# Kernel tuning notes

Measured on AMD Instinct MI355X. Metric: run time of the kernel, lower is better.

## Reference

```python
import jax, jax.numpy as jnp
import numpy as np

D_MODEL = 1024
N_HEADS = 16
D_HEAD = D_MODEL // N_HEADS
QLEN = 512
MLEN = 512
BATCH = 8


def setup_inputs() -> dict:
    key = jax.random.key(0)
    ks = jax.random.split(key, 12)
    s = 0.02
    inputs = jax.random.normal(ks[0], (QLEN, BATCH, D_MODEL), jnp.float32)
    r = jax.random.normal(ks[1], (QLEN + MLEN, 1, D_MODEL), jnp.float32)
    u = jax.random.normal(ks[2], (N_HEADS, D_HEAD), jnp.float32) * s
    v = jax.random.normal(ks[3], (N_HEADS, D_HEAD), jnp.float32) * s
    mem = jax.random.normal(ks[4], (MLEN, BATCH, D_MODEL), jnp.float32)
    # attention params (Transformer-XL style): fused qkv, r-projection, output proj
    W_qkv = jax.random.normal(ks[5], (D_MODEL, 3 * D_MODEL), jnp.float32) * s
    W_r = jax.random.normal(ks[6], (D_MODEL, D_MODEL), jnp.float32) * s
    W_o = jax.random.normal(ks[7], (D_MODEL, D_MODEL), jnp.float32) * s
    # GRU params: input-hidden and hidden-hidden for gates (r, z, n), torch layout
    W_ih = jax.random.normal(ks[8], (3 * D_MODEL, D_MODEL), jnp.float32) * s
    W_hh = jax.random.normal(ks[9], (3 * D_MODEL, D_MODEL), jnp.float32) * s
    b_ih = jax.random.normal(ks[10], (3 * D_MODEL,), jnp.float32) * s
    b_hh = jax.random.normal(ks[11], (3 * D_MODEL,), jnp.float32) * s
    h0 = jnp.zeros((BATCH, D_MODEL), jnp.float32)
    return dict(inputs=inputs, r=r, u=u, v=v, mem=mem, W_qkv=W_qkv, W_r=W_r,
                W_o=W_o, W_ih=W_ih, W_hh=W_hh, b_ih=b_ih, b_hh=b_hh, h0=h0)


def _rel_shift(x):
    # x: [q, k, b, h] -> Transformer-XL relative shift
    q, k, b, h = x.shape
    zero_pad = jnp.zeros((q, 1, b, h), x.dtype)
    x_padded = jnp.concatenate([zero_pad, x], axis=1)        # [q, k+1, b, h]
    x_padded = x_padded.reshape(k + 1, q, b, h)
    return x_padded[1:].reshape(q, k, b, h)


def _attention(inputs, r, u, v, mem, W_qkv, W_r, W_o):
    qlen, bsz, _ = inputs.shape
    cat = jnp.concatenate([mem, inputs], axis=0)             # [klen, b, d]
    klen = cat.shape[0]
    qkv = cat @ W_qkv                                        # [klen, b, 3d]
    w_head_q, w_head_k, w_head_v = jnp.split(qkv, 3, axis=-1)
    w_head_q = w_head_q[-qlen:]                              # [q, b, d]
    r_head_k = (r[:, 0, :] @ W_r).reshape(klen, N_HEADS, D_HEAD)  # [k, h, dh]

    q_ = w_head_q.reshape(qlen, bsz, N_HEADS, D_HEAD)
    k_ = w_head_k.reshape(klen, bsz, N_HEADS, D_HEAD)
    v_ = w_head_v.reshape(klen, bsz, N_HEADS, D_HEAD)

    AC = jnp.einsum('ibhd,jbhd->ijbh', q_ + u[None, None], k_)
    BD = jnp.einsum('ibhd,jhd->ijbh', q_ + v[None, None], r_head_k)
    BD = _rel_shift(BD)
    scale = 1.0 / np.sqrt(D_HEAD)
    attn_score = (AC + BD) * scale                           # [q, k, b, h]

    # causal mask with memory: query i attends to keys j <= i + mlen
    mlen = klen - qlen
    i = jnp.arange(qlen)[:, None]
    j = jnp.arange(klen)[None, :]
    mask = j > (i + mlen)                                    # [q, k]
    attn_score = jnp.where(mask[:, :, None, None], -jnp.inf, attn_score)

    attn_prob = jax.nn.softmax(attn_score, axis=1)
    attn_vec = jnp.einsum('ijbh,jbhd->ibhd', attn_prob, v_)
    attn_vec = attn_vec.reshape(qlen, bsz, D_MODEL)
    return attn_vec @ W_o                                    # [q, b, d]


def _gru(x, h0, W_ih, W_hh, b_ih, b_hh):
    # x: [T, B, D]; torch GRU cell math
    Wi_r, Wi_z, Wi_n = jnp.split(W_ih, 3, axis=0)
    Wh_r, Wh_z, Wh_n = jnp.split(W_hh, 3, axis=0)
    bi_r, bi_z, bi_n = jnp.split(b_ih, 3)
    bh_r, bh_z, bh_n = jnp.split(b_hh, 3)

    # precompute input projections for all timesteps
    xr = x @ Wi_r.T + bi_r
    xz = x @ Wi_z.T + bi_z
    xn = x @ Wi_n.T + bi_n

    def step(h, xs):
        xr_t, xz_t, xn_t = xs
        r = jax.nn.sigmoid(xr_t + h @ Wh_r.T + bh_r)
        z = jax.nn.sigmoid(xz_t + h @ Wh_z.T + bh_z)
        n = jnp.tanh(xn_t + r * (h @ Wh_n.T + bh_n))
        h_new = (1.0 - z) * n + z * h
        return h_new, h_new

    _, ys = jax.lax.scan(step, h0, (xr, xz, xn))
    return ys                                                # [T, B, D]


def reference(inputs, r, u, v, mem, W_qkv, W_r, W_o, W_ih, W_hh, b_ih, b_hh, h0):
    y = _attention(inputs, r, u, v, mem, W_qkv, W_r, W_o)
    return _gru(y, h0, W_ih, W_hh, b_ih, b_hh)
```

## Files before the change

kernel.cpp:

```cpp
#include <hip/hip_runtime.h>
#include <math.h>


typedef short bf16x8 __attribute__((ext_vector_type(8)));
typedef float f32x4 __attribute__((ext_vector_type(4)));

union FragU { uint4 u; bf16x8 h; };

__device__ inline void split2(float x0, float x1, unsigned& hi, unsigned& lo) {
    unsigned u0 = __float_as_uint(x0), u1 = __float_as_uint(x1);
    float h0 = __uint_as_float(u0 & 0xffff0000u);
    float h1 = __uint_as_float(u1 & 0xffff0000u);
    unsigned l0 = __float_as_uint(x0 - h0), l1 = __float_as_uint(x1 - h1);
    hi = (u0 >> 16) | (u1 & 0xffff0000u);
    lo = (l0 >> 16) | (l1 & 0xffff0000u);
}

__device__ __forceinline__ unsigned long long ld_coh64(const void* p) {
    return __hip_atomic_load((const unsigned long long*)p, __ATOMIC_RELAXED,
                             __HIP_MEMORY_SCOPE_AGENT);
}
__device__ __forceinline__ void st_coh64(void* p, unsigned long long v) {
    __hip_atomic_store((unsigned long long*)p, v, __ATOMIC_RELAXED,
                       __HIP_MEMORY_SCOPE_AGENT);
}

__device__ __forceinline__ void gl_lds16(const uint4* g, uint4* l) {
    __builtin_amdgcn_global_load_lds(
        (const __attribute__((address_space(1))) uint4*)g,
        (__attribute__((address_space(3))) uint4*)l, 16, 0, 0);
}

template<bool TR>
__global__ __launch_bounds__(256) void prep_w(
    const float* __restrict__ W, unsigned* __restrict__ out, int Nr, int K, int ldw)
{
    int idx = blockIdx.x * 256 + threadIdx.x;
    int cpr = K >> 3;
    if (idx >= Nr * cpr) return;
    int n, c;
    if (TR) { n = idx % Nr; c = idx / Nr; }
    else    { c = idx % cpr; n = idx / cpr; }
    int kt = c >> 2, j = c & 3;
    int k = kt * 32 + j * 8;
    float x[8];
    #pragma unroll
    for (int i = 0; i < 8; ++i)
        x[i] = TR ? W[(size_t)(k + i) * ldw + n] : W[(size_t)n * ldw + k + i];
    unsigned h[4], l[4];
    split2(x[0], x[1], h[0], l[0]);
    split2(x[2], x[3], h[1], l[1]);
    split2(x[4], x[5], h[2], l[2]);
    split2(x[6], x[7], h[3], l[3]);
    unsigned* base = out + (size_t)n * K + kt * 32;
    *(uint4*)(base + (((2 * j) ^ (n & 7)) * 4))     = make_uint4(h[0], h[1], h[2], h[3]);
    *(uint4*)(base + (((2 * j + 1) ^ (n & 7)) * 4)) = make_uint4(l[0], l[1], l[2], l[3]);
}

__global__ __launch_bounds__(256) void prep_cat(
    const float* __restrict__ mem, const float* __restrict__ inputs,
    unsigned* __restrict__ out)
{
    int idx = blockIdx.x * 256 + threadIdx.x;
    if (idx >= 1048576) return;
    int c = idx & 127, n = idx >> 7;
    int kt = c >> 2, j = c & 3;
    int k = kt * 32 + j * 8;
    const float* src = (n < 4096) ? (mem + (size_t)n * 1024 + k)
                                  : (inputs + (size_t)(n - 4096) * 1024 + k);
    float4 x0 = *(const float4*)src, x1 = *(const float4*)(src + 4);
    unsigned h[4], l[4];
    split2(x0.x, x0.y, h[0], l[0]);
    split2(x0.z, x0.w, h[1], l[1]);
    split2(x1.x, x1.y, h[2], l[2]);
    split2(x1.z, x1.w, h[3], l[3]);
    unsigned* base = out + (size_t)n * 1024 + kt * 32;
    *(uint4*)(base + (((2 * j) ^ (n & 7)) * 4))     = make_uint4(h[0], h[1], h[2], h[3]);
    *(uint4*)(base + (((2 * j + 1) ^ (n & 7)) * 4)) = make_uint4(l[0], l[1], l[2], l[3]);
}

template<bool BIAS>
__global__ __launch_bounds__(256) void gemm_pp(
    const uint4* __restrict__ Ap4, const uint4* __restrict__ Bp4,
    const float* __restrict__ bias, float* __restrict__ C, int K, int ldc)
{
    __shared__ uint4 Ab[1024];
    __shared__ uint4 Bb[1024];
    int tid = threadIdx.x;
    int lane = tid & 63, wid = tid >> 6;
    int wr = wid >> 1, wc = wid & 1;
    int n0 = blockIdx.x * 128, m0 = blockIdx.y * 128;
    int r15 = lane & 15, s = lane >> 4;
    int K4 = K >> 2;

    f32x4 acc[4][4];
    #pragma unroll
    for (int i = 0; i < 4; ++i)
        #pragma unroll
        for (int j = 0; j < 4; ++j) acc[i][j] = 0.0f;

    for (int kt = 0; kt < (K >> 5); ++kt) {
        #pragma unroll
        for (int q = 0; q < 4; ++q) {
            int base = q * 256 + wid * 64;
            int idx  = base + lane;
            int row = idx >> 3, slot = idx & 7;
            gl_lds16(Ap4 + (size_t)(m0 + row) * K4 + kt * 8 + slot, &Ab[base]);
            gl_lds16(Bp4 + (size_t)(n0 + row) * K4 + kt * 8 + slot, &Bb[base]);
        }
        __syncthreads();
        FragU ahi[4], alo[4], bhi[4], blo[4];
        #pragma unroll
        for (int f = 0; f < 4; ++f) {
            int ar = wr * 64 + f * 16 + r15;
            ahi[f].u = Ab[ar * 8 + ((2 * s) ^ (ar & 7))];
            alo[f].u = Ab[ar * 8 + ((2 * s + 1) ^ (ar & 7))];
            int br = wc * 64 + f * 16 + r15;
            bhi[f].u = Bb[br * 8 + ((2 * s) ^ (br & 7))];
            blo[f].u = Bb[br * 8 + ((2 * s + 1) ^ (br & 7))];
        }
        #pragma unroll
        for (int fi = 0; fi < 4; ++fi)
            #pragma unroll
            for (int fj = 0; fj < 4; ++fj) {
                acc[fi][fj] = __builtin_amdgcn_mfma_f32_16x16x32_bf16(ahi[fi].h, bhi[fj].h, acc[fi][fj], 0, 0, 0);
                acc[fi][fj] = __builtin_amdgcn_mfma_f32_16x16x32_bf16(ahi[fi].h, blo[fj].h, acc[fi][fj], 0, 0, 0);
                acc[fi][fj] = __builtin_amdgcn_mfma_f32_16x16x32_bf16(alo[fi].h, bhi[fj].h, acc[fi][fj], 0, 0, 0);
            }
        __syncthreads();
    }
    int r4 = (lane >> 4) * 4;
    #pragma unroll
    for (int fj = 0; fj < 4; ++fj) {
        int n = n0 + wc * 64 + fj * 16 + r15;
        float bv = BIAS ? bias[n] : 0.f;
        #pragma unroll
        for (int fi = 0; fi < 4; ++fi) {
            int m = m0 + wr * 64 + fi * 16 + r4;
            #pragma unroll
            for (int r = 0; r < 4; ++r)
                C[(size_t)(m + r) * ldc + n] = acc[fi][fj][r] + bv;
        }
    }
}

template<int AMODE, bool BIAS>
__global__ __launch_bounds__(256) void gemm_mfma(
    const float* __restrict__ A, const float* __restrict__ A2,
    const unsigned* __restrict__ Bp, const float* __restrict__ bias,
    float* __restrict__ C, int M, int N, int K, int lda, int ldc)
{
    __shared__ uint4 Ab[1024];
    __shared__ uint4 Bb[1024];
    int tid = threadIdx.x;
    int lane = tid & 63, wid = tid >> 6;
    int wr = wid >> 1, wc = wid & 1;
    int n0 = blockIdx.x * 128, m0 = blockIdx.y * 128;
    int r15 = lane & 15, s = lane >> 4;

    f32x4 acc[4][4];
    #pragma unroll
    for (int i = 0; i < 4; ++i)
        #pragma unroll
        for (int j = 0; j < 4; ++j) acc[i][j] = 0.0f;

    for (int kt = 0; kt < (K >> 5); ++kt) {
        int k0 = kt * 32;
        #pragma unroll
        for (int q = 0; q < 2; ++q) {
            int idx = q * 256 + tid;
            int row = idx >> 2, j = idx & 3;
            const float* ap;
            if (AMODE == 1) {
                int gm = m0 + row;
                ap = (gm < 4096) ? (A + (size_t)gm * lda) : (A2 + (size_t)(gm - 4096) * lda);
            } else {
                ap = A + (size_t)(m0 + row) * lda;
            }
            float4 x0 = *(const float4*)(ap + k0 + j * 8);
            float4 x1 = *(const float4*)(ap + k0 + j * 8 + 4);
            unsigned h[4], l[4];
            split2(x0.x, x0.y, h[0], l[0]);
            split2(x0.z, x0.w, h[1], l[1]);
            split2(x1.x, x1.y, h[2], l[2]);
            split2(x1.z, x1.w, h[3], l[3]);
            Ab[row * 8 + (((2 * j) ^ (row & 7)))]     = make_uint4(h[0], h[1], h[2], h[3]);
            Ab[row * 8 + (((2 * j + 1) ^ (row & 7)))] = make_uint4(l[0], l[1], l[2], l[3]);
        }
        #pragma unroll
        for (int q = 0; q < 4; ++q) {
            int idx = q * 256 + tid;
            int row = idx >> 3, slot = idx & 7;
            Bb[idx] = *(const uint4*)(Bp + (size_t)(n0 + row) * K + k0 + slot * 4);
        }
        __syncthreads();
        FragU ahi[4], alo[4], bhi[4], blo[4];
        #pragma unroll
        for (int f = 0; f < 4; ++f) {
            int ar = wr * 64 + f * 16 + r15;
            ahi[f].u = Ab[ar * 8 + ((2 * s) ^ (ar & 7))];
            alo[f].u = Ab[ar * 8 + ((2 * s + 1) ^ (ar & 7))];
            int br = wc * 64 + f * 16 + r15;
            bhi[f].u = Bb[br * 8 + ((2 * s) ^ (br & 7))];
            blo[f].u = Bb[br * 8 + ((2 * s + 1) ^ (br & 7))];
        }
        #pragma unroll
        for (int fi = 0; fi < 4; ++fi)
            #pragma unroll
            for (int fj = 0; fj < 4; ++fj) {
                acc[fi][fj] = __builtin_amdgcn_mfma_f32_16x16x32_bf16(ahi[fi].h, bhi[fj].h, acc[fi][fj], 0, 0, 0);
                acc[fi][fj] = __builtin_amdgcn_mfma_f32_16x16x32_bf16(ahi[fi].h, blo[fj].h, acc[fi][fj], 0, 0, 0);
                acc[fi][fj] = __builtin_amdgcn_mfma_f32_16x16x32_bf16(alo[fi].h, bhi[fj].h, acc[fi][fj], 0, 0, 0);
            }
        __syncthreads();
    }
    int r4 = (lane >> 4) * 4;
    #pragma unroll
    for (int fj = 0; fj < 4; ++fj) {
        int n = n0 + wc * 64 + fj * 16 + r15;
        float bv = BIAS ? bias[n] : 0.f;
        #pragma unroll
        for (int fi = 0; fi < 4; ++fi) {
            int m = m0 + wr * 64 + fi * 16 + r4;
            #pragma unroll
            for (int r = 0; r < 4; ++r)
                C[(size_t)(m + r) * ldc + n] = acc[fi][fj][r] + bv;
        }
    }
}

__global__ __launch_bounds__(256) void attn_fused(
    const float* __restrict__ qkv, const float* __restrict__ rk,
    const float* __restrict__ u_, const float* __restrict__ v_,
    float* __restrict__ y1)
{
    __shared__ float qu[64][68], qv[64][68], Kt[64][68], Vt[64][68];
    __shared__ float RKs[128][68];
    __shared__ float S[64][68];
    __shared__ float mrow[64], lrow[64], scalef[64];
    __shared__ float pmax[64][16], psum[64][16];

    int tid = threadIdx.x;
    int it = blockIdx.x, b = blockIdx.y, h = blockIdx.z;
    int i0 = it * 64;
    int ti = tid >> 4, tj = tid & 15;

    {
        int r = tid >> 2, c0 = (tid & 3) * 16;
        size_t base = ((size_t)(i0 + r + 512) * 8 + b) * 3072 + h * 64;
        #pragma unroll
        for (int q = 0; q < 4; ++q) {
            int c = c0 + q * 4;
            float4 qq = *(const float4*)&qkv[base + c];
            float4 uu = *(const float4*)&u_[h * 64 + c];
            float4 vv = *(const float4*)&v_[h * 64 + c];
            *(float4*)&qu[r][c] = make_float4(qq.x + uu.x, qq.y + uu.y, qq.z + uu.z, qq.w + uu.w);
            *(float4*)&qv[r][c] = make_float4(qq.x + vv.x, qq.y + vv.y, qq.z + vv.z, qq.w + vv.w);
        }
    }
    if (tid < 64) { mrow[tid] = -1e30f; lrow[tid] = 0.f; }

    float Od[4][4] = {};
    int njt = it + 9;

    for (int jt = 0; jt < njt; ++jt) {
        int j0 = jt * 64;
        __syncthreads();
        {
            int r = tid >> 2, c0 = (tid & 3) * 16;
            size_t kb = ((size_t)(j0 + r) * 8 + b) * 3072 + 1024 + h * 64;
            #pragma unroll
            for (int q = 0; q < 4; ++q) {
                int c = c0 + q * 4;
                *(float4*)&Kt[r][c] = *(const float4*)&qkv[kb + c];
                *(float4*)&Vt[r][c] = *(const float4*)&qkv[kb + 1024 + c];
            }
        }
        {
            int r2 = tid >> 1, c0 = (tid & 1) * 32;
            int jj = j0 - i0 + 448 + r2;
            jj = jj < 0 ? 0 : (jj > 1023 ? 1023 : jj);
            size_t rb = (size_t)jj * 1024 + h * 64;
            #pragma unroll
            for (int q = 0; q < 8; ++q) {
                int c = c0 + q * 4;
                *(float4*)&RKs[r2][c] = *(const float4*)&rk[rb + c];
            }
        }
        __syncthreads();

        float acc[4][4] = {};
        int jlb = (tj - ti) * 4 + 60;
        #pragma unroll 4
        for (int d4 = 0; d4 < 64; d4 += 4) {
            float4 Aq[4], Cq[4], Kv[4], Rv[7];
            #pragma unroll
            for (int i = 0; i < 4; ++i) {
                Aq[i] = *(float4*)&qu[ti * 4 + i][d4];
                Cq[i] = *(float4*)&qv[ti * 4 + i][d4];
                Kv[i] = *(float4*)&Kt[tj * 4 + i][d4];
            }
            #pragma unroll
            for (int t = 0; t < 7; ++t)
                Rv[t] = *(float4*)&RKs[jlb + t][d4];
            #pragma unroll
            for (int i = 0; i < 4; ++i)
                #pragma unroll
                for (int j = 0; j < 4; ++j) {
                    float4 kk = Kv[j];
                    float4 rr = Rv[j - i + 3];
                    acc[i][j] += Aq[i].x * kk.x + Aq[i].y * kk.y + Aq[i].z * kk.z + Aq[i].w * kk.w
                               + Cq[i].x * rr.x + Cq[i].y * rr.y + Cq[i].z * rr.z + Cq[i].w * rr.w;
                }
        }
        #pragma unroll
        for (int i = 0; i < 4; ++i) {
            int gi = i0 + ti * 4 + i;
            float mx = -1e30f;
            #pragma unroll
            for (int j = 0; j < 4; ++j) {
                int gj = j0 + tj * 4 + j;
                float vS = acc[i][j] * 0.125f;
                if (gj > gi + 512) vS = -1e30f;
                acc[i][j] = vS;
                mx = fmaxf(mx, vS);
            }
            pmax[ti * 4 + i][tj] = mx;
        }
        __syncthreads();
        if (tid < 64) {
            float mo = mrow[tid], mn = mo;
            #pragma unroll
            for (int t = 0; t < 16; ++t) mn = fmaxf(mn, pmax[tid][t]);
            mrow[tid] = mn;
            scalef[tid] = __expf(mo - mn);
        }
        __syncthreads();
        #pragma unroll
        for (int i = 0; i < 4; ++i) {
            int ri = ti * 4 + i;
            float mn = mrow[ri];
            float4 pv;
            pv.x = __expf(acc[i][0] - mn);
            pv.y = __expf(acc[i][1] - mn);
            pv.z = __expf(acc[i][2] - mn);
            pv.w = __expf(acc[i][3] - mn);
            *(float4*)&S[ri][tj * 4] = pv;
            psum[ri][tj] = pv.x + pv.y + pv.z + pv.w;
            float scl = scalef[ri];
            #pragma unroll
            for (int j2 = 0; j2 < 4; ++j2) Od[i][j2] *= scl;
        }
        __syncthreads();
        if (tid < 64) {
            float s = 0.f;
            #pragma unroll
            for (int t = 0; t < 16; ++t) s += psum[tid][t];
            lrow[tid] = lrow[tid] * scalef[tid] + s;
        }
        #pragma unroll 4
        for (int jb = 0; jb < 64; jb += 4) {
            float4 p0 = *(float4*)&S[ti * 4 + 0][jb];
            float4 p1 = *(float4*)&S[ti * 4 + 1][jb];
            float4 p2 = *(float4*)&S[ti * 4 + 2][jb];
            float4 p3 = *(float4*)&S[ti * 4 + 3][jb];
            float4 v0 = *(float4*)&Vt[jb + 0][tj * 4];
            float4 v1 = *(float4*)&Vt[jb + 1][tj * 4];
            float4 v2 = *(float4*)&Vt[jb + 2][tj * 4];
            float4 v3 = *(float4*)&Vt[jb + 3][tj * 4];
            float4 pr[4] = {p0, p1, p2, p3};
            #pragma unroll
            for (int i = 0; i < 4; ++i) {
                Od[i][0] += pr[i].x * v0.x + pr[i].y * v1.x + pr[i].z * v2.x + pr[i].w * v3.x;
                Od[i][1] += pr[i].x * v0.y + pr[i].y * v1.y + pr[i].z * v2.y + pr[i].w * v3.y;
                Od[i][2] += pr[i].x * v0.z + pr[i].y * v1.z + pr[i].z * v2.z + pr[i].w * v3.z;
                Od[i][3] += pr[i].x * v0.w + pr[i].y * v1.w + pr[i].z * v2.w + pr[i].w * v3.w;
            }
        }
    }
    __syncthreads();
    #pragma unroll
    for (int i = 0; i < 4; ++i) {
        int ri = ti * 4 + i;
        float inv = 1.f / lrow[ri];
        float4 o = make_float4(Od[i][0] * inv, Od[i][1] * inv, Od[i][2] * inv, Od[i][3] * inv);
        *(float4*)&y1[((size_t)(i0 + ri) * 8 + b) * 1024 + h * 64 + tj * 4] = o;
    }
}

__global__ __launch_bounds__(256) void prep_whh(
    const float* __restrict__ Whh, uint4* __restrict__ outp)
{
    int idx = blockIdx.x * 256 + threadIdx.x;
    if (idx >= 393216) return;
    int lane = idx & 63;
    int rest = idx >> 6;
    int gate = rest % 3;
    int kt   = (rest / 3) & 31;
    int g64  = rest / 96;
    int n = gate * 1024 + g64 * 16 + (lane & 15);
    int k = kt * 32 + (lane >> 4) * 8;
    const float* src = Whh + (size_t)n * 1024 + k;
    float4 x0 = *(const float4*)src, x1 = *(const float4*)(src + 4);
    unsigned h[4], l[4];
    split2(x0.x, x0.y, h[0], l[0]);
    split2(x0.z, x0.w, h[1], l[1]);
    split2(x1.x, x1.y, h[2], l[2]);
    split2(x1.z, x1.w, h[3], l[3]);
    outp[((size_t)rest * 2 + 0) * 64 + lane] = make_uint4(h[0], h[1], h[2], h[3]);
    outp[((size_t)rest * 2 + 1) * 64 + lane] = make_uint4(l[0], l[1], l[2], l[3]);
}

__global__ __launch_bounds__(256, 1) void gru_persist2(
    const float* __restrict__ h0, float* __restrict__ hA, float* __restrict__ hB,
    const uint4* __restrict__ WhhG, const float* __restrict__ bhh,
    const float* __restrict__ xg, float* __restrict__ out,
    unsigned* __restrict__ flags)
{
    __shared__ uint4 Bf[4096];
    __shared__ float red[3][64][4];
    int tid = threadIdx.x;
    int lane = tid & 63, wv = tid >> 6;
    int g64 = blockIdx.x;

    int col = lane & 15;
    int d0 = g64 * 16 + (lane >> 4) * 4;
    bool act = (wv == 0) && (col < 8);
    float4 br4 = make_float4(0, 0, 0, 0), bz4 = br4, bn4 = br4;
    if (act) {
        br4 = *(const float4*)&bhh[d0];
        bz4 = *(const float4*)&bhh[1024 + d0];
        bn4 = *(const float4*)&bhh[2048 + d0];
    }
    const uint4* wb = WhhG + (size_t)g64 * 12288 + (wv < 3 ? wv : 0) * 128 + lane;

    for (int t = 0; t < 512; ++t) {
        const float* hi_ = (t == 0) ? h0 : ((t & 1) ? hA : hB);
        float* ho = (t & 1) ? hB : hA;

        float4 xr4, xz4, xn4;
        unsigned long long hp01 = 0, hp23 = 0;
        if (act) {
            size_t xb = ((size_t)t * 8 + col) * 3072 + d0;
            xr4 = *(const float4*)&xg[xb];
            xz4 = *(const float4*)&xg[xb + 1024];
            xn4 = *(const float4*)&xg[xb + 2048];
            hp01 = ld_coh64(hi_ + col * 1024 + d0);
            hp23 = ld_coh64(hi_ + col * 1024 + d0 + 2);
        }

        uint4 wA[16], wB[16];
        #pragma unroll
        for (int q = 0; q < 8; ++q) {
            wA[2 * q]     = wb[q * 384];
            wA[2 * q + 1] = wb[q * 384 + 64];
        }

        unsigned long long hq[16];
        #pragma unroll
        for (int i = 0; i < 4; ++i) {
            int s = i * 256 + tid;
            const float* hp = hi_ + (s & 7) * 1024 + (s >> 5) * 32 + ((s >> 3) & 3) * 8;
            #pragma unroll
            for (int q = 0; q < 4; ++q) hq[i * 4 + q] = ld_coh64(hp + q * 2);
        }
        #pragma unroll
        for (int i = 0; i < 4; ++i) {
            int s = i * 256 + tid;
            int b = s & 7, oct = (s >> 3) & 3, kt = s >> 5;
            float x[8];
            #pragma unroll
            for (int q = 0; q < 4; ++q) {
                x[2 * q]     = __uint_as_float((unsigned)(hq[i * 4 + q] & 0xffffffffu));
                x[2 * q + 1] = __uint_as_float((unsigned)(hq[i * 4 + q] >> 32));
            }
            unsigned hh[4], ll[4];
            split2(x[0], x[1], hh[0], ll[0]);
            split2(x[2], x[3], hh[1], ll[1]);
            split2(x[4], x[5], hh[2], ll[2]);
            split2(x[6], x[7], hh[3], ll[3]);
            int ln = oct * 16 + b;
            Bf[(kt * 2 + 0) * 64 + ln] = make_uint4(hh[0], hh[1], hh[2], hh[3]);
            Bf[(kt * 2 + 1) * 64 + ln] = make_uint4(ll[0], ll[1], ll[2], ll[3]);
        }
        __syncthreads();

        f32x4 acc = 0.0f;
        #define GRU_LOAD(dst, c0)                                   \
            _Pragma("unroll")                                       \
            for (int q = 0; q < 8; ++q) {                           \
                dst[2 * q]     = wb[((c0) * 8 + q) * 384];          \
                dst[2 * q + 1] = wb[((c0) * 8 + q) * 384 + 64];     \
            }
        #define GRU_COMP(src, c0)                                   \
            _Pragma("unroll")                                       \
            for (int q = 0; q < 8; ++q) {                           \
                int kt = (c0) * 8 + q;                              \
                FragU ah, al, bh, bl;                               \
                ah.u = src[2 * q]; al.u = src[2 * q + 1];           \
                bh.u = Bf[(kt * 2 + 0) * 64 + lane];                \
                bl.u = Bf[(kt * 2 + 1) * 64 + lane];                \
                acc = __builtin_amdgcn_mfma_f32_16x16x32_bf16(ah.h, bh.h, acc, 0, 0, 0); \
                acc = __builtin_amdgcn_mfma_f32_16x16x32_bf16(ah.h, bl.h, acc, 0, 0, 0); \
                acc = __builtin_amdgcn_mfma_f32_16x16x32_bf16(al.h, bh.h, acc, 0, 0, 0); \
            }
        if (wv < 3) {
            GRU_LOAD(wB, 1);
            GRU_COMP(wA, 0);
            GRU_LOAD(wA, 2);
            GRU_COMP(wB, 1);
            GRU_LOAD(wB, 3);
            GRU_COMP(wA, 2);
            GRU_COMP(wB, 3);
            *(f32x4*)&red[wv][lane][0] = acc;
        }
        #undef GRU_LOAD
        #undef GRU_COMP
        __syncthreads();

        if (act) {
            f32x4 aR = *(f32x4*)&red[0][lane][0];
            f32x4 aZ = *(f32x4*)&red[1][lane][0];
            f32x4 aN = *(f32x4*)&red[2][lane][0];
            float xr[4] = {xr4.x, xr4.y, xr4.z, xr4.w};
            float xz[4] = {xz4.x, xz4.y, xz4.z, xz4.w};
            float xn[4] = {xn4.x, xn4.y, xn4.z, xn4.w};
            float hp[4] = {__uint_as_float((unsigned)(hp01 & 0xffffffffu)),
                           __uint_as_float((unsigned)(hp01 >> 32)),
                           __uint_as_float((unsigned)(hp23 & 0xffffffffu)),
                           __uint_as_float((unsigned)(hp23 >> 32))};
            float br[4] = {br4.x, br4.y, br4.z, br4.w};
            float bz[4] = {bz4.x, bz4.y, bz4.z, bz4.w};
            float bn[4] = {bn4.x, bn4.y, bn4.z, bn4.w};
            float hn[4];
            #pragma unroll
            for (int r = 0; r < 4; ++r) {
                float rr = 1.f / (1.f + __expf(-(xr[r] + aR[r] + br[r])));
                float zz = 1.f / (1.f + __expf(-(xz[r] + aZ[r] + bz[r])));
                float nn = tanhf(xn[r] + rr * (aN[r] + bn[r]));
                hn[r] = (1.f - zz) * nn + zz * hp[r];
            }
            unsigned long long v01 = (unsigned long long)__float_as_uint(hn[0])
                                   | ((unsigned long long)__float_as_uint(hn[1]) << 32);
            unsigned long long v23 = (unsigned long long)__float_as_uint(hn[2])
                                   | ((unsigned long long)__float_as_uint(hn[3]) << 32);
            st_coh64(ho + col * 1024 + d0, v01);
            st_coh64(ho + col * 1024 + d0 + 2, v23);
            *(float4*)&out[((size_t)t * 8 + col) * 1024 + d0] =
                make_float4(hn[0], hn[1], hn[2], hn[3]);
        }

        if (t != 511) {
            __syncthreads();
            unsigned tgt = (unsigned)t + 1u;
            if (tid < 64) {
                if (tid == 0)
                    __hip_atomic_store(&flags[(size_t)g64 * 16], tgt,
                                       __ATOMIC_RELAXED, __HIP_MEMORY_SCOPE_AGENT);
                const unsigned* fp = &flags[(size_t)tid * 16];
                for (;;) {
                    unsigned f = __hip_atomic_load(fp, __ATOMIC_RELAXED,
                                                   __HIP_MEMORY_SCOPE_AGENT);
                    if (__all(f >= tgt)) break;
                }
            }
            __syncthreads();
        }
    }
}

__global__ __launch_bounds__(192, 1) void gru_step_mfma(
    const float* __restrict__ hin, float* __restrict__ hout,
    const uint4* __restrict__ WhhG, const float* __restrict__ bhh,
    const float* __restrict__ xg, float* __restrict__ out, int t)
{
    __shared__ uint4 Bf[4096];
    __shared__ float red[3][64][4];
    int tid = threadIdx.x;
    int lane = tid & 63, wv = tid >> 6;
    int g64 = blockIdx.x;

    int col = lane & 15;
    int d0 = g64 * 16 + (lane >> 4) * 4;
    bool act = (wv == 0) && (col < 8);
    float4 xr4, xz4, xn4, hp4, br4, bz4, bn4;
    if (act) {
        size_t xb = ((size_t)t * 8 + col) * 3072 + d0;
        xr4 = *(const float4*)&xg[xb];
        xz4 = *(const float4*)&xg[xb + 1024];
        xn4 = *(const float4*)&xg[xb + 2048];
        hp4 = *(const float4*)&hin[col * 1024 + d0];
        br4 = *(const float4*)&bhh[d0];
        bz4 = *(const float4*)&bhh[1024 + d0];
        bn4 = *(const float4*)&bhh[2048 + d0];
    }

    const uint4* wb = WhhG + (size_t)g64 * 12288 + wv * 128 + lane;
    uint4 wA[16], wB[16];
    #pragma unroll
    for (int q = 0; q < 8; ++q) {
        wA[2 * q]     = wb[q * 384];
        wA[2 * q + 1] = wb[q * 384 + 64];
    }

    for (int s = tid; s < 1024; s += 192) {
        int b = s & 7, oct = (s >> 3) & 3, kt = s >> 5;
        const float* hp = hin + b * 1024 + kt * 32 + oct * 8;
        float4 x0 = *(const float4*)hp, x1 = *(const float4*)(hp + 4);
        unsigned hh[4], ll[4];
        split2(x0.x, x0.y, hh[0], ll[0]);
        split2(x0.z, x0.w, hh[1], ll[1]);
        split2(x1.x, x1.y, hh[2], ll[2]);
        split2(x1.z, x1.w, hh[3], ll[3]);
        int ln = oct * 16 + b;
        Bf[(kt * 2 + 0) * 64 + ln] = make_uint4(hh[0], hh[1], hh[2], hh[3]);
        Bf[(kt * 2 + 1) * 64 + ln] = make_uint4(ll[0], ll[1], ll[2], ll[3]);
    }
    __syncthreads();

    f32x4 acc = 0.0f;
    #define GRU_LOAD(dst, c0)                                   \
        _Pragma("unroll")                                       \
        for (int q = 0; q < 8; ++q) {                           \
            dst[2 * q]     = wb[((c0) * 8 + q) * 384];          \
            dst[2 * q + 1] = wb[((c0) * 8 + q) * 384 + 64];     \
        }
    #define GRU_COMP(src, c0)                                   \
        _Pragma("unroll")                                       \
        for (int q = 0; q < 8; ++q) {                           \
            int kt = (c0) * 8 + q;                              \
            FragU ah, al, bh, bl;                               \
            ah.u = src[2 * q]; al.u = src[2 * q + 1];           \
            bh.u = Bf[(kt * 2 + 0) * 64 + lane];                \
            bl.u = Bf[(kt * 2 + 1) * 64 + lane];                \
            acc = __builtin_amdgcn_mfma_f32_16x16x32_bf16(ah.h, bh.h, acc, 0, 0, 0); \
            acc = __builtin_amdgcn_mfma_f32_16x16x32_bf16(ah.h, bl.h, acc, 0, 0, 0); \
            acc = __builtin_amdgcn_mfma_f32_16x16x32_bf16(al.h, bh.h, acc, 0, 0, 0); \
        }
    GRU_LOAD(wB, 1);
    GRU_COMP(wA, 0);
    GRU_LOAD(wA, 2);
    GRU_COMP(wB, 1);
    GRU_LOAD(wB, 3);
    GRU_COMP(wA, 2);
    GRU_COMP(wB, 3);
    #undef GRU_LOAD
    #undef GRU_COMP

    *(f32x4*)&red[wv][lane][0] = acc;
    __syncthreads();

    if (act) {
        f32x4 aR = *(f32x4*)&red[0][lane][0];
        f32x4 aZ = *(f32x4*)&red[1][lane][0];
        f32x4 aN = *(f32x4*)&red[2][lane][0];
        float xr[4] = {xr4.x, xr4.y, xr4.z, xr4.w};
        float xz[4] = {xz4.x, xz4.y, xz4.z, xz4.w};
        float xn[4] = {xn4.x, xn4.y, xn4.z, xn4.w};
        float hp[4] = {hp4.x, hp4.y, hp4.z, hp4.w};
        float br[4] = {br4.x, br4.y, br4.z, br4.w};
        float bz[4] = {bz4.x, bz4.y, bz4.z, bz4.w};
        float bn[4] = {bn4.x, bn4.y, bn4.z, bn4.w};
        float hn[4];
        #pragma unroll
        for (int r = 0; r < 4; ++r) {
            float rr = 1.f / (1.f + __expf(-(xr[r] + aR[r] + br[r])));
            float zz = 1.f / (1.f + __expf(-(xz[r] + aZ[r] + bz[r])));
            float nn = tanhf(xn[r] + rr * (aN[r] + bn[r]));
            hn[r] = (1.f - zz) * nn + zz * hp[r];
        }
        float4 hv = make_float4(hn[0], hn[1], hn[2], hn[3]);
        *(float4*)&hout[col * 1024 + d0] = hv;
        *(float4*)&out[((size_t)t * 8 + col) * 1024 + d0] = hv;
    }
}

extern "C" void kernel_launch(void* const* d_in, const int* in_sizes, int n_in,
                              void* d_out, int out_size, void* d_ws, size_t ws_size,
                              hipStream_t stream) {
    (void)in_sizes; (void)n_in; (void)out_size; (void)ws_size;
    const float* inputs = (const float*)d_in[0];
    const float* r_in   = (const float*)d_in[1];
    const float* u_in   = (const float*)d_in[2];
    const float* v_in   = (const float*)d_in[3];
    const float* mem    = (const float*)d_in[4];
    const float* Wqkv   = (const float*)d_in[5];
    const float* Wr     = (const float*)d_in[6];
    const float* Wo     = (const float*)d_in[7];
    const float* Wih    = (const float*)d_in[8];
    const float* Whh    = (const float*)d_in[9];
    const float* bih    = (const float*)d_in[10];
    const float* bhh    = (const float*)d_in[11];
    const float* h0     = (const float*)d_in[12];
    float* out = (float*)d_out;
    float* ws = (float*)d_ws;

    float*    qkv   = ws;
    float*    rk    = ws + 25165824;
    float*    y1    = ws + 26214400;
    float*    y2    = ws + 30408704;
    float*    xg    = ws + 34603008;
    float*    hA    = ws + 47185920;
    float*    hB    = ws + 47194112;
    unsigned* WqkvP = (unsigned*)(ws + 47202304);
    unsigned* WrP   = (unsigned*)(ws + 50348032);
    unsigned* WoP   = (unsigned*)(ws + 51396608);
    unsigned* WihP  = (unsigned*)(ws + 52445184);
    unsigned* flags = (unsigned*)(ws + 55590912);
    uint4*    WhhG  = (uint4*)qkv;
    unsigned* y1P   = (unsigned*)(qkv + 4194304);
    unsigned* y2P   = (unsigned*)(qkv + 8388608);
    unsigned* catP  = (unsigned*)xg;

    dim3 blk(256);
    prep_w<true ><<<1536, blk, 0, stream>>>(Wqkv, WqkvP, 3072, 1024, 3072);
    prep_w<true ><<< 512, blk, 0, stream>>>(Wr,   WrP,   1024, 1024, 1024);
    prep_w<true ><<< 512, blk, 0, stream>>>(Wo,   WoP,   1024, 1024, 1024);
    prep_w<false><<<1536, blk, 0, stream>>>(Wih,  WihP,  3072, 1024, 1024);
    hipMemsetAsync(flags, 0, 4096, stream);

    prep_cat<<<4096, blk, 0, stream>>>(mem, inputs, catP);
    gemm_pp<false><<<dim3(24, 64), blk, 0, stream>>>(
        (const uint4*)catP, (const uint4*)WqkvP, nullptr, qkv, 1024, 3072);
    gemm_mfma<0, false><<<dim3(8, 8), blk, 0, stream>>>(
        r_in, nullptr, WrP, nullptr, rk, 1024, 1024, 1024, 1024, 1024);
    attn_fused<<<dim3(8, 8, 16), blk, 0, stream>>>(qkv, rk, u_in, v_in, y1);
    prep_whh<<<1536, blk, 0, stream>>>(Whh, WhhG);
    prep_w<false><<<2048, blk, 0, stream>>>(y1, y1P, 4096, 1024, 1024);
    gemm_pp<false><<<dim3(8, 32), blk, 0, stream>>>(
        (const uint4*)y1P, (const uint4*)WoP, nullptr, y2, 1024, 1024);
    prep_w<false><<<2048, blk, 0, stream>>>(y2, y2P, 4096, 1024, 1024);
    gemm_pp<true><<<dim3(24, 32), blk, 0, stream>>>(
        (const uint4*)y2P, (const uint4*)WihP, bih, xg, 1024, 3072);

    {
        const float* a0 = h0; float* a1 = hA; float* a2 = hB;
        const uint4* a3 = WhhG; const float* a4 = bhh; const float* a5 = xg;
        float* a6 = out; unsigned* a7 = flags;
        void* args[8] = {&a0, &a1, &a2, &a3, &a4, &a5, &a6, &a7};
        hipError_t e = hipLaunchCooperativeKernel((void*)gru_persist2,
                                                  dim3(64), dim3(256), args, 0, stream);
        if (e != hipSuccess) {
            const float* hin = h0;
            for (int s = 0; s < 512; ++s) {
                float* hp = (s & 1) ? hB : hA;
                gru_step_mfma<<<64, dim3(192), 0, stream>>>(hin, hp, WhhG, bhh, xg, out, s);
                hin = hp;
            }
        }
    }
}
```

Before: 4.719 ms.

## Fuse bf16 split packing into attention and Wo GEMM epilogues, skip unused QKV work

The attention kernel now writes its output directly in the packed hi/lo bf16 swizzled layout, and the Wo GEMM gains a SPLITOUT epilogue that stages results through shared memory and emits packed output. This removes the two standalone prep_w conversion passes and their intermediate fp32 round trips. The QKV GEMM is split so memory rows compute only K/V columns, skipping the unused Q projection for the memory part. The cost is extra shared-memory syncs in the epilogue and scattered 8-byte stores in attention.

New measurement: 4.701 ms. Within noise of the previous version (-0.4%).

```diff
diff --git a/kernel.cpp b/kernel.cpp
--- a/kernel.cpp
+++ b/kernel.cpp
@@ -79,18 +79,21 @@
     *(uint4*)(base + (((2 * j + 1) ^ (n & 7)) * 4)) = make_uint4(l[0], l[1], l[2], l[3]);
 }
 
-template<bool BIAS>
+template<bool BIAS, bool SPLITOUT>
 __global__ __launch_bounds__(256) void gemm_pp(
     const uint4* __restrict__ Ap4, const uint4* __restrict__ Bp4,
-    const float* __restrict__ bias, float* __restrict__ C, int K, int ldc)
+    const float* __restrict__ bias, float* __restrict__ C,
+    unsigned* __restrict__ Cp, int K, int ldc)
 {
-    __shared__ uint4 Ab[1024];
-    __shared__ uint4 Bb[1024];
+    __shared__ uint4 SH[2048];
+    uint4* Ab = SH;
+    uint4* Bb = SH + 1024;
     int tid = threadIdx.x;
     int lane = tid & 63, wid = tid >> 6;
     int wr = wid >> 1, wc = wid & 1;
     int n0 = blockIdx.x * 128, m0 = blockIdx.y * 128;
     int r15 = lane & 15, s = lane >> 4;
+    int r4 = (lane >> 4) * 4;
     int K4 = K >> 2;
 
     f32x4 acc[4][4];
@@ -129,17 +132,53 @@
             }
         __syncthreads();
     }
-    int r4 = (lane >> 4) * 4;
-    #pragma unroll
-    for (int fj = 0; fj < 4; ++fj) {
-        int n = n0 + wc * 64 + fj * 16 + r15;
-        float bv = BIAS ? bias[n] : 0.f;
-        #pragma unroll
-        for (int fi = 0; fi < 4; ++fi) {
-            int m = m0 + wr * 64 + fi * 16 + r4;
-            #pragma unroll
-            for (int r = 0; r < 4; ++r)
-                C[(size_t)(m + r) * ldc + n] = acc[fi][fj][r] + bv;
+
+    if (!SPLITOUT) {
+        #pragma unroll
+        for (int fj = 0; fj < 4; ++fj) {
+            int n = n0 + wc * 64 + fj * 16 + r15;
+            float bv = BIAS ? bias[n] : 0.f;
+            #pragma unroll
+            for (int fi = 0; fi < 4; ++fi) {
+                int m = m0 + wr * 64 + fi * 16 + r4;
+                #pragma unroll
+                for (int r = 0; r < 4; ++r)
+                    C[(size_t)(m + r) * ldc + n] = acc[fi][fj][r] + bv;
+            }
+        }
+    } else {
+        float* Cs = (float*)SH;
+        #pragma unroll
+        for (int half = 0; half < 2; ++half) {
+            __syncthreads();
+            if (wr == half) {
+                #pragma unroll
+                for (int fi = 0; fi < 4; ++fi)
+                    #pragma unroll
+                    for (int fj = 0; fj < 4; ++fj)
+                        #pragma unroll
+                        for (int r = 0; r < 4; ++r)
+                            Cs[(fi * 16 + r4 + r) * 128 + wc * 64 + fj * 16 + r15] = acc[fi][fj][r];
+            }
+            __syncthreads();
+            #pragma unroll
+            for (int q = 0; q < 4; ++q) {
+                int oc = q * 256 + tid;
+                int lr = oc >> 4, oct = oc & 15;
+                float4 xa = *(float4*)&Cs[lr * 128 + oct * 8];
+                float4 xb = *(float4*)&Cs[lr * 128 + oct * 8 + 4];
+                unsigned hw[4], lw[4];
+                split2(xa.x, xa.y, hw[0], lw[0]);
+                split2(xa.z, xa.w, hw[1], lw[1]);
+                split2(xb.x, xb.y, hw[2], lw[2]);
+                split2(xb.z, xb.w, hw[3], lw[3]);
+                int m = m0 + half * 64 + lr;
+                int k = n0 + oct * 8;
+                int kt2 = k >> 5, j2 = (k >> 3) & 3;
+                unsigned* bp = Cp + (size_t)m * ldc + kt2 * 32;
+                *(uint4*)(bp + (((2 * j2)     ^ (m & 7)) * 4)) = make_uint4(hw[0], hw[1], hw[2], hw[3]);
+                *(uint4*)(bp + (((2 * j2 + 1) ^ (m & 7)) * 4)) = make_uint4(lw[0], lw[1], lw[2], lw[3]);
+            }
         }
     }
 }
@@ -232,7 +271,7 @@
 __global__ __launch_bounds__(256) void attn_fused(
     const float* __restrict__ qkv, const float* __restrict__ rk,
     const float* __restrict__ u_, const float* __restrict__ v_,
-    float* __restrict__ y1)
+    unsigned* __restrict__ y1P)
 {
     __shared__ float qu[64][68], qv[64][68], Kt[64][68], Vt[64][68];
     __shared__ float RKs[128][68];
@@ -384,7 +423,16 @@
         int ri = ti * 4 + i;
         float inv = 1.f / lrow[ri];
         float4 o = make_float4(Od[i][0] * inv, Od[i][1] * inv, Od[i][2] * inv, Od[i][3] * inv);
-        *(float4*)&y1[((size_t)(i0 + ri) * 8 + b) * 1024 + h * 64 + tj * 4] = o;
+        int n = (i0 + ri) * 8 + b;
+        unsigned hw0, hw1, lw0, lw1;
+        split2(o.x, o.y, hw0, lw0);
+        split2(o.z, o.w, hw1, lw1);
+        int kt2 = 2 * h + (tj >> 3);
+        int j2 = (tj >> 1) & 3;
+        int wo = (tj & 1) * 2;
+        unsigned* bp = y1P + (size_t)n * 1024 + kt2 * 32;
+        *(uint2*)(bp + (((2 * j2)     ^ (n & 7)) * 4) + wo) = make_uint2(hw0, hw1);
+        *(uint2*)(bp + (((2 * j2 + 1) ^ (n & 7)) * 4) + wo) = make_uint2(lw0, lw1);
     }
 }
 
@@ -697,8 +745,8 @@
 
     float*    qkv   = ws;
     float*    rk    = ws + 25165824;
-    float*    y1    = ws + 26214400;
-    float*    y2    = ws + 30408704;
+    unsigned* y1P   = (unsigned*)(ws + 26214400);
+    unsigned* y2P   = (unsigned*)(ws + 30408704);
     float*    xg    = ws + 34603008;
     float*    hA    = ws + 47185920;
     float*    hB    = ws + 47194112;
@@ -708,8 +756,6 @@
     unsigned* WihP  = (unsigned*)(ws + 52445184);
     unsigned* flags = (unsigned*)(ws + 55590912);
     uint4*    WhhG  = (uint4*)qkv;
-    unsigned* y1P   = (unsigned*)(qkv + 4194304);
-    unsigned* y2P   = (unsigned*)(qkv + 8388608);
     unsigned* catP  = (unsigned*)xg;
 
     dim3 blk(256);
@@ -720,18 +766,20 @@
     hipMemsetAsync(flags, 0, 4096, stream);
 
     prep_cat<<<4096, blk, 0, stream>>>(mem, inputs, catP);
-    gemm_pp<false><<<dim3(24, 64), blk, 0, stream>>>(
-        (const uint4*)catP, (const uint4*)WqkvP, nullptr, qkv, 1024, 3072);
+    gemm_pp<false, false><<<dim3(16, 32), blk, 0, stream>>>(
+        (const uint4*)catP, (const uint4*)WqkvP + 1024 * 256, nullptr,
+        qkv + 1024, nullptr, 1024, 3072);
+    gemm_pp<false, false><<<dim3(24, 32), blk, 0, stream>>>(
+        (const uint4*)catP + 4096 * 256, (const uint4*)WqkvP, nullptr,
+        qkv + (size_t)4096 * 3072, nullptr, 1024, 3072);
     gemm_mfma<0, false><<<dim3(8, 8), blk, 0, stream>>>(
         r_in, nullptr, WrP, nullptr, rk, 1024, 1024, 1024, 1024, 1024);
-    attn_fused<<<dim3(8, 8, 16), blk, 0, stream>>>(qkv, rk, u_in, v_in, y1);
+    attn_fused<<<dim3(8, 8, 16), blk, 0, stream>>>(qkv, rk, u_in, v_in, y1P);
     prep_whh<<<1536, blk, 0, stream>>>(Whh, WhhG);
-    prep_w<false><<<2048, blk, 0, stream>>>(y1, y1P, 4096, 1024, 1024);
-    gemm_pp<false><<<dim3(8, 32), blk, 0, stream>>>(
-        (const uint4*)y1P, (const uint4*)WoP, nullptr, y2, 1024, 1024);
-    prep_w<false><<<2048, blk, 0, stream>>>(y2, y2P, 4096, 1024, 1024);
-    gemm_pp<true><<<dim3(24, 32), blk, 0, stream>>>(
-        (const uint4*)y2P, (const uint4*)WihP, bih, xg, 1024, 3072);
+    gemm_pp<false, true><<<dim3(8, 32), blk, 0, stream>>>(
+        (const uint4*)y1P, (const uint4*)WoP, nullptr, nullptr, y2P, 1024, 1024);
+    gemm_pp<true, false><<<dim3(24, 32), blk, 0, stream>>>(
+        (const uint4*)y2P, (const uint4*)WihP, bih, xg, nullptr, 1024, 3072);
 
     {
         const float* a0 = h0; float* a1 = hA; float* a2 = hB;
```
